# Kernel optimization log

Hardware: AMD Instinct MI355X
Metric: run time of the kernel (lower is better)

Reference implementation:

```python
import jax, jax.numpy as jnp
import numpy as np

EPS = 1e-5


def _binary_act(x):
    # Forward: sign(x). Backward: piecewise-polynomial surrogate (ApproxSign STE).
    out3 = jnp.where(x < -1, -1.0,
            jnp.where(x < 0, x * x + 2.0 * x,
             jnp.where(x < 1, -x * x + 2.0 * x, 1.0)))
    return jax.lax.stop_gradient(jnp.sign(x) - out3) + out3


def _binarize_weights(w):
    # Per-output-channel scaling factor (detached), forward = scale*sign(w),
    # backward flows through clamp(w, -1, 1) (STE).
    scale = jax.lax.stop_gradient(jnp.mean(jnp.abs(w), axis=(1, 2, 3), keepdims=True))
    clipped = jnp.clip(w, -1.0, 1.0)
    return jax.lax.stop_gradient(scale * jnp.sign(w) - clipped) + clipped


def setup_inputs() -> dict:
    key = jax.random.key(0)
    kx, kw = jax.random.split(key)
    B, Cin, Cout, H, W = 32, 128, 128, 56, 56
    x = jax.random.normal(kx, (B, Cin, H, W), dtype=jnp.float32)
    # HardBinaryConv: weight = rand(n)*0.001 permuted then reshaped -> just random in [0, 0.001)
    w = jax.random.uniform(kw, (Cout, Cin, 3, 3), dtype=jnp.float32) * 0.001
    return {
        "x": x,
        "bias0": jnp.zeros((Cin,), jnp.float32),   # move0 LearnableBias
        "w": w,                                     # HardBinaryConv latent weights
        "gamma": jnp.ones((Cout,), jnp.float32),    # BN weight
        "beta": jnp.zeros((Cout,), jnp.float32),    # BN bias
        "bias1": jnp.zeros((Cout,), jnp.float32),   # move1
        "alpha": jnp.full((Cout,), 0.25, jnp.float32),  # PReLU per-channel
        "bias2": jnp.zeros((Cout,), jnp.float32),   # move2
    }


def reference(x, bias0, w, gamma, beta, bias1, alpha, bias2):
    def pc(v):  # per-channel broadcast (1, C, 1, 1)
        return v[None, :, None, None]

    residual = x
    out = x + pc(bias0)                     # move0
    out = _binary_act(out)                  # binary activation
    bw = _binarize_weights(w)               # {-scale, +scale} weights
    y = jax.lax.conv_general_dilated(
        out, bw, window_strides=(1, 1), padding=((1, 1), (1, 1)),
        dimension_numbers=("NCHW", "OIHW", "NCHW"))
    # BatchNorm2d (training mode: biased batch statistics over N,H,W)
    mean = jnp.mean(y, axis=(0, 2, 3), keepdims=True)
    var = jnp.mean(jnp.square(y - mean), axis=(0, 2, 3), keepdims=True)
    y = (y - mean) * jax.lax.rsqrt(var + EPS) * pc(gamma) + pc(beta)
    y = y + residual
    y = y + pc(bias1)                       # move1
    y = jnp.where(y >= 0, y, pc(alpha) * y)  # PReLU
    y = y + pc(bias2)                       # move2
    return y
```

## Files before the change

### kernel.cpp

```cpp
#include <hip/hip_runtime.h>
#include <stdint.h>

#define NB 32
#define NC 128
#define NH 56
#define NW 56
#define NHW_ (NH * NW)
#define NPIX (NB * NHW_)
#define NO 128
#define NK 1152
#define ROWPAIRS (NH / 2)

typedef unsigned long long u64;

__global__ __launch_bounds__(256) void pack_act(const float* __restrict__ x,
                                                const float* __restrict__ bias0,
                                                u64* __restrict__ packA) {
    int p = blockIdx.x * 256 + threadIdx.x;
    if (p >= NPIX) return;
    int n = p / NHW_;
    int rem = p - n * NHW_;
    const float* xb = x + (size_t)n * NC * NHW_ + rem;
    u64 w0 = 0, w1 = 0;
#pragma unroll 8
    for (int c = 0; c < 64; ++c)
        w0 |= (u64)((xb[(size_t)c * NHW_] + bias0[c]) > 0.f) << c;
#pragma unroll 8
    for (int c = 0; c < 64; ++c)
        w1 |= (u64)((xb[(size_t)(c + 64) * NHW_] + bias0[c + 64]) > 0.f) << c;
    packA[(size_t)p * 2]     = w0;
    packA[(size_t)p * 2 + 1] = w1;
}

__global__ __launch_bounds__(64) void pack_wgt(const float* __restrict__ w,
                                               u64* __restrict__ packW,
                                               float* __restrict__ scaleW) {
    int o = blockIdx.x;
    int t = threadIdx.x;
    const float* wo = w + (size_t)o * NK;
    float s = 0.f;
    for (int i = t; i < NK; i += 64) s += fabsf(wo[i]);
    for (int off = 32; off; off >>= 1) s += __shfl_down(s, off);
    if (t == 0) scaleW[o] = s / (float)NK;
    if (t < 18) {
        int tap = t >> 1;
        int j   = t & 1;
        u64 bits = 0;
        for (int cc = 0; cc < 64; ++cc) {
            int c = j * 64 + cc;
            bits |= (u64)(wo[c * 9 + tap] > 0.f) << cc;
        }
        packW[((size_t)o * 9 + tap) * 2 + j] = bits;
    }
}

__global__ __launch_bounds__(256) void conv_bin(const u64* __restrict__ packA,
                                                const u64* __restrict__ packW,
                                                short* __restrict__ yI) {
    __shared__ u64 lw[NO * 18];
    for (int i = threadIdx.x; i < NO * 18; i += 256) lw[i] = packW[i];

    int bid = blockIdx.x;
    int n = bid / ROWPAIRS, hp = bid - n * ROWPAIRS;
    int h0 = hp * 2;
    int wave = threadIdx.x >> 6, lane = threadIdx.x & 63;
    bool act = lane < NW;

    u64 a[4][3][2];
    bool rv[4], cv[3];
#pragma unroll
    for (int r = 0; r < 4; ++r) {
        int hi = h0 - 1 + r;
        rv[r] = (hi >= 0) && (hi < NH);
    }
    cv[0] = act && (lane >= 1);
    cv[1] = act;
    cv[2] = act && (lane + 1 < NW);
#pragma unroll
    for (int r = 0; r < 4; ++r) {
        int hi = h0 - 1 + r;
        int hc = hi < 0 ? 0 : (hi >= NH ? NH - 1 : hi);
#pragma unroll
        for (int c = 0; c < 3; ++c) {
            int wi = lane - 1 + c;
            int wc = wi < 0 ? 0 : (wi >= NW ? NW - 1 : wi);
            size_t idx = ((size_t)n * NHW_ + (size_t)hc * NW + wc) * 2;
            ulonglong2 q = *reinterpret_cast<const ulonglong2*>(packA + idx);
            bool v = rv[r] && cv[c];
            a[r][c][0] = v ? q.x : 0;
            a[r][c][1] = v ? q.y : 0;
        }
    }
    __syncthreads();

    short* yrow = yI + (size_t)n * NO * NHW_ + (size_t)h0 * NW + lane;

    for (int oo = 0; oo < 32; ++oo) {
        int o = (wave << 5) + oo;
        const u64* wp = &lw[o * 18];
        int dot0 = 0, dot1 = 0;
#pragma unroll
        for (int kh = 0; kh < 3; ++kh) {
#pragma unroll
            for (int kw = 0; kw < 3; ++kw) {
                int t = kh * 3 + kw;
                u64 w0 = wp[2 * t], w1 = wp[2 * t + 1];
                int pc0 = __popcll(a[kh][kw][0] ^ w0) + __popcll(a[kh][kw][1] ^ w1);
                int pc1 = __popcll(a[kh + 1][kw][0] ^ w0) + __popcll(a[kh + 1][kw][1] ^ w1);
                dot0 += (rv[kh] && cv[kw]) ? (NC - 2 * pc0) : 0;
                dot1 += (rv[kh + 1] && cv[kw]) ? (NC - 2 * pc1) : 0;
            }
        }
        if (act) {
            yrow[(size_t)o * NHW_]      = (short)dot0;
            yrow[(size_t)o * NHW_ + NW] = (short)dot1;
        }
    }
}

__global__ __launch_bounds__(256) void stats_y(const short* __restrict__ yI,
                                               int* __restrict__ sumP,
                                               u64* __restrict__ sqP) {
    int b = blockIdx.x;
    int o = b >> 2, q = b & 3;
    long long s = 0, sq = 0;
    for (int v = threadIdx.x; v < 3136; v += 256) {
        int nl = v / 392, off = v - nl * 392;
        int n = q * 8 + nl;
        const int4 pv = *reinterpret_cast<const int4*>(
            yI + ((size_t)n * NO + o) * NHW_ + (size_t)off * 8);
        int qs[4] = {pv.x, pv.y, pv.z, pv.w};
#pragma unroll
        for (int j = 0; j < 4; ++j) {
            int lo = (int)(short)(qs[j] & 0xffff);
            int hi = (int)(qs[j] >> 16);
            s += lo + hi;
            sq += (long long)(lo * lo + hi * hi);
        }
    }
    __shared__ long long ls[256];
    __shared__ long long lq[256];
    int tid = threadIdx.x;
    ls[tid] = s; lq[tid] = sq;
    __syncthreads();
    for (int st = 128; st; st >>= 1) {
        if (tid < st) { ls[tid] += ls[tid + st]; lq[tid] += lq[tid + st]; }
        __syncthreads();
    }
    if (tid == 0) {
        sumP[o * 4 + q] = (int)ls[0];
        sqP[o * 4 + q]  = (u64)lq[0];
    }
}

__global__ __launch_bounds__(128) void bn_coef(const int* __restrict__ sumP,
                                               const u64* __restrict__ sqP,
                                               const float* __restrict__ scaleW,
                                               const float* __restrict__ gamma,
                                               const float* __restrict__ beta,
                                               const float* __restrict__ bias1,
                                               float* __restrict__ coefA,
                                               float* __restrict__ coefB,
                                               int nparts) {
    int o = threadIdx.x;
    long long si = 0; u64 qi = 0;
    for (int k = 0; k < nparts; ++k) {
        si += sumP[o * nparts + k];
        qi += sqP[o * nparts + k];
    }
    double cnt = (double)NPIX;
    double mean = (double)si / cnt;
    double var = (double)qi / cnt - mean * mean;
    if (var < 0.0) var = 0.0;
    float sc = scaleW[o];
    float rs = rsqrtf((float)((double)sc * (double)sc * var) + 1e-5f);
    float g = gamma[o];
    float a = sc * g * rs;
    float b = beta[o] - (float)((double)sc * mean) * g * rs;
    coefA[o] = a;
    coefB[o] = b + bias1[o];
}

__global__ __launch_bounds__(256) void final_store(const short* __restrict__ yI,
                                                   const float* __restrict__ x,
                                                   const float* __restrict__ coefA,
                                                   const float* __restrict__ coefB,
                                                   const float* __restrict__ alpha,
                                                   const float* __restrict__ bias2,
                                                   float* __restrict__ out) {
    const size_t ngroups = (size_t)NB * NO * NHW_ / 8;
    for (size_t g = (size_t)blockIdx.x * blockDim.x + threadIdx.x; g < ngroups;
         g += (size_t)gridDim.x * blockDim.x) {
        size_t i = g * 8;
        int o = (int)((i / NHW_) % NO);
        float a = coefA[o], bb = coefB[o], al = alpha[o], b2 = bias2[o];
        int4 yv = *reinterpret_cast<const int4*>(yI + i);
        float4 x0 = *reinterpret_cast<const float4*>(x + i);
        float4 x1 = *reinterpret_cast<const float4*>(x + i + 4);
        int q[4] = {yv.x, yv.y, yv.z, yv.w};
        float xs[8] = {x0.x, x0.y, x0.z, x0.w, x1.x, x1.y, x1.z, x1.w};
        float r[8];
#pragma unroll
        for (int j = 0; j < 4; ++j) {
            float lo = (float)(short)(q[j] & 0xffff);
            float hi = (float)(q[j] >> 16);
            float t0 = fmaf(a, lo, bb) + xs[2 * j];
            float t1 = fmaf(a, hi, bb) + xs[2 * j + 1];
            t0 = t0 >= 0.f ? t0 : al * t0;
            t1 = t1 >= 0.f ? t1 : al * t1;
            r[2 * j]     = t0 + b2;
            r[2 * j + 1] = t1 + b2;
        }
        float4 o0 = {r[0], r[1], r[2], r[3]};
        float4 o1 = {r[4], r[5], r[6], r[7]};
        *reinterpret_cast<float4*>(out + i)     = o0;
        *reinterpret_cast<float4*>(out + i + 4) = o1;
    }
}

__device__ inline void load_nbhd(const u64* __restrict__ packA, int n, int h,
                                 int wcol, bool act, u64 a[9][2], unsigned* vmask) {
    unsigned m = 0;
#pragma unroll
    for (int kh = 0; kh < 3; ++kh) {
        int hi = h + kh - 1;
        bool vh = (hi >= 0) && (hi < NH);
#pragma unroll
        for (int kw = 0; kw < 3; ++kw) {
            int wi = wcol + kw - 1;
            int t = kh * 3 + kw;
            bool v = act && vh && (wi >= 0) && (wi < NW);
            int hc = hi < 0 ? 0 : (hi >= NH ? NH - 1 : hi);
            int wc = wi < 0 ? 0 : (wi >= NW ? NW - 1 : wi);
            size_t idx = ((size_t)n * NHW_ + (size_t)hc * NW + wc) * 2;
            u64 q0 = packA[idx], q1 = packA[idx + 1];
            a[t][0] = v ? q0 : 0;
            a[t][1] = v ? q1 : 0;
            m |= (unsigned)v << t;
        }
    }
    *vmask = m;
}

__global__ __launch_bounds__(256) void conv_stats_atomic(const u64* __restrict__ packA,
                                                         const u64* __restrict__ packW,
                                                         int* __restrict__ sumI,
                                                         u64* __restrict__ sumsqI) {
    __shared__ u64 lw[NO * 18];
    for (int i = threadIdx.x; i < NO * 18; i += 256) lw[i] = packW[i];
    int nh = blockIdx.x;
    int n = nh / NH, h = nh - n * NH;
    int wave = threadIdx.x >> 6, lane = threadIdx.x & 63;
    bool act = lane < NW;
    u64 a[9][2]; unsigned vm;
    load_nbhd(packA, n, h, lane, act, a, &vm);
    __syncthreads();
    for (int oo = 0; oo < 32; ++oo) {
        int o = (wave << 5) + oo;
        int dot = 0;
#pragma unroll
        for (int t = 0; t < 9; ++t) {
            int pc = __popcll(a[t][0] ^ lw[(o * 9 + t) * 2]) +
                     __popcll(a[t][1] ^ lw[(o * 9 + t) * 2 + 1]);
            dot += ((vm >> t) & 1) ? (NC - 2 * pc) : 0;
        }
        int s = dot, sq = dot * dot;
        for (int off = 32; off; off >>= 1) {
            s  += __shfl_down(s, off);
            sq += __shfl_down(sq, off);
        }
        if (lane == 0) {
            atomicAdd(&sumI[o], s);
            atomicAdd(&sumsqI[o], (u64)(unsigned)sq);
        }
    }
}

__global__ __launch_bounds__(256) void final_recompute(const u64* __restrict__ packA,
                                                       const u64* __restrict__ packW,
                                                       const float* __restrict__ coefA,
                                                       const float* __restrict__ coefB,
                                                       const float* __restrict__ alpha,
                                                       const float* __restrict__ bias2,
                                                       const float* __restrict__ x,
                                                       float* __restrict__ out) {
    __shared__ u64 lw[NO * 18];
    for (int i = threadIdx.x; i < NO * 18; i += 256) lw[i] = packW[i];
    int nh = blockIdx.x;
    int n = nh / NH, h = nh - n * NH;
    int wave = threadIdx.x >> 6, lane = threadIdx.x & 63;
    bool act = lane < NW;
    u64 a[9][2]; unsigned vm;
    load_nbhd(packA, n, h, lane, act, a, &vm);
    __syncthreads();
    for (int oo = 0; oo < 32; ++oo) {
        int o = (wave << 5) + oo;
        int dot = 0;
#pragma unroll
        for (int t = 0; t < 9; ++t) {
            int pc = __popcll(a[t][0] ^ lw[(o * 9 + t) * 2]) +
                     __popcll(a[t][1] ^ lw[(o * 9 + t) * 2 + 1]);
            dot += ((vm >> t) & 1) ? (NC - 2 * pc) : 0;
        }
        if (act) {
            size_t idx = ((size_t)n * NO + o) * NHW_ + (size_t)h * NW + lane;
            float t = fmaf(coefA[o], (float)dot, coefB[o]) + x[idx];
            t = t >= 0.f ? t : alpha[o] * t;
            out[idx] = t + bias2[o];
        }
    }
}

extern "C" void kernel_launch(void* const* d_in, const int* in_sizes, int n_in,
                              void* d_out, int out_size, void* d_ws, size_t ws_size,
                              hipStream_t stream) {
    (void)in_sizes; (void)n_in; (void)out_size;
    const float* x     = (const float*)d_in[0];
    const float* bias0 = (const float*)d_in[1];
    const float* w     = (const float*)d_in[2];
    const float* gamma = (const float*)d_in[3];
    const float* beta  = (const float*)d_in[4];
    const float* bias1 = (const float*)d_in[5];
    const float* alpha = (const float*)d_in[6];
    const float* bias2 = (const float*)d_in[7];
    float* out = (float*)d_out;
    char* ws = (char*)d_ws;

    u64*   packA  = (u64*)ws;
    u64*   packW  = (u64*)(ws + 1605632);
    float* scaleW = (float*)(ws + 1624064);
    int*   sumP   = (int*)(ws + 1624576);
    u64*   sqP    = (u64*)(ws + 1626624);
    float* coefA  = (float*)(ws + 1630720);
    float* coefB  = (float*)(ws + 1631232);
    short* yI     = (short*)(ws + 1631744);
    bool store = ws_size >= (size_t)1631744 + (size_t)NB * NO * NHW_ * 2;

    pack_act<<<NPIX / 256, 256, 0, stream>>>(x, bias0, packA);
    pack_wgt<<<NO, 64, 0, stream>>>(w, packW, scaleW);

    if (store) {
        conv_bin<<<NB * ROWPAIRS, 256, 0, stream>>>(packA, packW, yI);
        stats_y<<<NO * 4, 256, 0, stream>>>(yI, sumP, sqP);
        bn_coef<<<1, NO, 0, stream>>>(sumP, sqP, scaleW, gamma, beta, bias1, coefA, coefB, 4);
        final_store<<<2048, 256, 0, stream>>>(yI, x, coefA, coefB, alpha, bias2, out);
    } else {
        hipMemsetAsync(sumP, 0, 2048 + 4096, stream);
        conv_stats_atomic<<<NB * NH, 256, 0, stream>>>(packA, packW, sumP, sqP);
        bn_coef<<<1, NO, 0, stream>>>(sumP, sqP, scaleW, gamma, beta, bias1, coefA, coefB, 1);
        final_recompute<<<NB * NH, 256, 0, stream>>>(packA, packW, coefA, coefB, alpha, bias2, x, out);
    }
}
```

Measured before the change: 105.3 us.

## Compute four output rows per thread with precomputed padding corrections

The binary conv kernel now processes 4-row strips per block, split across two 64-channel halves, so each loaded activation neighbourhood serves four output rows. Per-tap masking is replaced by unmasked popcounts and a fixed border correction precomputed per output channel in pack_wgt. The separate stats and bn_coef kernels are merged into one per-channel kernel, which removes a launch but drops the 4-way split of the statistics work. More registers are needed for the 6x3 neighbourhood, and occupancy hint 4 is added.

```diff
diff --git a/kernel.cpp b/kernel.cpp
--- a/kernel.cpp
+++ b/kernel.cpp
@@ -9,7 +9,7 @@
 #define NPIX (NB * NHW_)
 #define NO 128
 #define NK 1152
-#define ROWPAIRS (NH / 2)
+#define NSTRIP 14
 
 typedef unsigned long long u64;
 
@@ -34,7 +34,9 @@
 
 __global__ __launch_bounds__(64) void pack_wgt(const float* __restrict__ w,
                                                u64* __restrict__ packW,
-                                               float* __restrict__ scaleW) {
+                                               float* __restrict__ scaleW,
+                                               int* __restrict__ corrW) {
+    __shared__ u64 sb[18];
     int o = blockIdx.x;
     int t = threadIdx.x;
     const float* wo = w + (size_t)o * NK;
@@ -50,83 +52,122 @@
             int c = j * 64 + cc;
             bits |= (u64)(wo[c * 9 + tap] > 0.f) << cc;
         }
-        packW[((size_t)o * 9 + tap) * 2 + j] = bits;
-    }
-}
-
-__global__ __launch_bounds__(256) void conv_bin(const u64* __restrict__ packA,
-                                                const u64* __restrict__ packW,
-                                                short* __restrict__ yI) {
-    __shared__ u64 lw[NO * 18];
-    for (int i = threadIdx.x; i < NO * 18; i += 256) lw[i] = packW[i];
+        packW[(size_t)o * 18 + t] = bits;
+        sb[t] = bits;
+    }
+    __syncthreads();
+    if (t == 0) {
+        int cv[9];
+#pragma unroll
+        for (int tap = 0; tap < 9; ++tap)
+            cv[tap] = NC - 2 * (__popcll(sb[2 * tap]) + __popcll(sb[2 * tap + 1]));
+        int* cw = corrW + o * 8;
+        cw[0] = cv[0] + cv[3] + cv[6];
+        cw[1] = cv[2] + cv[5] + cv[8];
+        cw[2] = cv[0] + cv[1] + cv[2];
+        cw[3] = cv[6] + cv[7] + cv[8];
+        cw[4] = cv[0];
+        cw[5] = cv[2];
+        cw[6] = cv[6];
+        cw[7] = cv[8];
+    }
+}
+
+__global__ __launch_bounds__(256, 4) void conv_bin(const u64* __restrict__ packA,
+                                                   const u64* __restrict__ packW,
+                                                   const int* __restrict__ corrW,
+                                                   short* __restrict__ yI) {
+    __shared__ u64 lw[64 * 18];
+    __shared__ int lc[64 * 8];
 
     int bid = blockIdx.x;
-    int n = bid / ROWPAIRS, hp = bid - n * ROWPAIRS;
-    int h0 = hp * 2;
-    int wave = threadIdx.x >> 6, lane = threadIdx.x & 63;
+    int n = bid / (NSTRIP * 2);
+    int rem = bid - n * (NSTRIP * 2);
+    int strip = rem >> 1;
+    int chh = rem & 1;
+    int obase = chh * 64;
+    int h0 = strip * 4;
+
+    for (int i = threadIdx.x; i < 64 * 18; i += 256) lw[i] = packW[(size_t)obase * 18 + i];
+    for (int i = threadIdx.x; i < 64 * 8; i += 256) lc[i] = corrW[obase * 8 + i];
+
+    int wv = threadIdx.x >> 6, lane = threadIdx.x & 63;
     bool act = lane < NW;
-
-    u64 a[4][3][2];
-    bool rv[4], cv[3];
-#pragma unroll
-    for (int r = 0; r < 4; ++r) {
+    bool top = (strip == 0), bot = (strip == NSTRIP - 1);
+
+    u64 a[6][3][2];
+    bool cvv[3];
+    cvv[0] = act && (lane >= 1);
+    cvv[1] = act;
+    cvv[2] = act && (lane + 1 < NW);
+#pragma unroll
+    for (int r = 0; r < 6; ++r) {
         int hi = h0 - 1 + r;
-        rv[r] = (hi >= 0) && (hi < NH);
-    }
-    cv[0] = act && (lane >= 1);
-    cv[1] = act;
-    cv[2] = act && (lane + 1 < NW);
-#pragma unroll
-    for (int r = 0; r < 4; ++r) {
-        int hi = h0 - 1 + r;
+        bool rvv = (hi >= 0) && (hi < NH);
         int hc = hi < 0 ? 0 : (hi >= NH ? NH - 1 : hi);
 #pragma unroll
         for (int c = 0; c < 3; ++c) {
             int wi = lane - 1 + c;
             int wc = wi < 0 ? 0 : (wi >= NW ? NW - 1 : wi);
-            size_t idx = ((size_t)n * NHW_ + (size_t)hc * NW + wc) * 2;
-            ulonglong2 q = *reinterpret_cast<const ulonglong2*>(packA + idx);
-            bool v = rv[r] && cv[c];
+            ulonglong2 q = *reinterpret_cast<const ulonglong2*>(
+                packA + ((size_t)n * NHW_ + (size_t)hc * NW + wc) * 2);
+            bool v = rvv && cvv[c];
             a[r][c][0] = v ? q.x : 0;
             a[r][c][1] = v ? q.y : 0;
         }
     }
     __syncthreads();
 
-    short* yrow = yI + (size_t)n * NO * NHW_ + (size_t)h0 * NW + lane;
-
-    for (int oo = 0; oo < 32; ++oo) {
-        int o = (wave << 5) + oo;
-        const u64* wp = &lw[o * 18];
-        int dot0 = 0, dot1 = 0;
+    bool isL = (lane == 0), isR = (lane == NW - 1);
+    short* ybase = yI + (size_t)n * NO * NHW_ + (size_t)h0 * NW + lane;
+
+    for (int oo = 0; oo < 16; ++oo) {
+        int lo = (wv << 4) + oo;
+        int o = obase + lo;
+        const u64* wp = &lw[lo * 18];
+        int pc0 = 0, pc1 = 0, pc2 = 0, pc3 = 0;
 #pragma unroll
         for (int kh = 0; kh < 3; ++kh) {
 #pragma unroll
             for (int kw = 0; kw < 3; ++kw) {
-                int t = kh * 3 + kw;
-                u64 w0 = wp[2 * t], w1 = wp[2 * t + 1];
-                int pc0 = __popcll(a[kh][kw][0] ^ w0) + __popcll(a[kh][kw][1] ^ w1);
-                int pc1 = __popcll(a[kh + 1][kw][0] ^ w0) + __popcll(a[kh + 1][kw][1] ^ w1);
-                dot0 += (rv[kh] && cv[kw]) ? (NC - 2 * pc0) : 0;
-                dot1 += (rv[kh + 1] && cv[kw]) ? (NC - 2 * pc1) : 0;
+                u64 w0 = wp[(kh * 3 + kw) * 2];
+                u64 w1 = wp[(kh * 3 + kw) * 2 + 1];
+                pc0 += __popcll(a[0 + kh][kw][0] ^ w0) + __popcll(a[0 + kh][kw][1] ^ w1);
+                pc1 += __popcll(a[1 + kh][kw][0] ^ w0) + __popcll(a[1 + kh][kw][1] ^ w1);
+                pc2 += __popcll(a[2 + kh][kw][0] ^ w0) + __popcll(a[2 + kh][kw][1] ^ w1);
+                pc3 += __popcll(a[3 + kh][kw][0] ^ w0) + __popcll(a[3 + kh][kw][1] ^ w1);
             }
         }
+        const int* cw = &lc[lo * 8];
+        int corrcol = isL ? cw[0] : (isR ? cw[1] : 0);
+        int base = NK - corrcol;
+        int d0 = base - 2 * pc0;
+        int d1 = base - 2 * pc1;
+        int d2 = base - 2 * pc2;
+        int d3 = base - 2 * pc3;
+        if (top) d0 -= cw[2] - (isL ? cw[4] : (isR ? cw[5] : 0));
+        if (bot) d3 -= cw[3] - (isL ? cw[6] : (isR ? cw[7] : 0));
         if (act) {
-            yrow[(size_t)o * NHW_]      = (short)dot0;
-            yrow[(size_t)o * NHW_ + NW] = (short)dot1;
-        }
-    }
-}
-
-__global__ __launch_bounds__(256) void stats_y(const short* __restrict__ yI,
-                                               int* __restrict__ sumP,
-                                               u64* __restrict__ sqP) {
-    int b = blockIdx.x;
-    int o = b >> 2, q = b & 3;
+            short* yp = ybase + (size_t)o * NHW_;
+            yp[0]      = (short)d0;
+            yp[NW]     = (short)d1;
+            yp[2 * NW] = (short)d2;
+            yp[3 * NW] = (short)d3;
+        }
+    }
+}
+
+__global__ __launch_bounds__(256) void stats_coef(const short* __restrict__ yI,
+                                                  const float* __restrict__ scaleW,
+                                                  const float* __restrict__ gamma,
+                                                  const float* __restrict__ beta,
+                                                  const float* __restrict__ bias1,
+                                                  float* __restrict__ coefA,
+                                                  float* __restrict__ coefB) {
+    int o = blockIdx.x;
     long long s = 0, sq = 0;
-    for (int v = threadIdx.x; v < 3136; v += 256) {
-        int nl = v / 392, off = v - nl * 392;
-        int n = q * 8 + nl;
+    for (int v = threadIdx.x; v < 12544; v += 256) {
+        int n = v / 392, off = v - n * 392;
         const int4 pv = *reinterpret_cast<const int4*>(
             yI + ((size_t)n * NO + o) * NHW_ + (size_t)off * 8);
         int qs[4] = {pv.x, pv.y, pv.z, pv.w};
@@ -148,37 +189,16 @@
         __syncthreads();
     }
     if (tid == 0) {
-        sumP[o * 4 + q] = (int)ls[0];
-        sqP[o * 4 + q]  = (u64)lq[0];
-    }
-}
-
-__global__ __launch_bounds__(128) void bn_coef(const int* __restrict__ sumP,
-                                               const u64* __restrict__ sqP,
-                                               const float* __restrict__ scaleW,
-                                               const float* __restrict__ gamma,
-                                               const float* __restrict__ beta,
-                                               const float* __restrict__ bias1,
-                                               float* __restrict__ coefA,
-                                               float* __restrict__ coefB,
-                                               int nparts) {
-    int o = threadIdx.x;
-    long long si = 0; u64 qi = 0;
-    for (int k = 0; k < nparts; ++k) {
-        si += sumP[o * nparts + k];
-        qi += sqP[o * nparts + k];
-    }
-    double cnt = (double)NPIX;
-    double mean = (double)si / cnt;
-    double var = (double)qi / cnt - mean * mean;
-    if (var < 0.0) var = 0.0;
-    float sc = scaleW[o];
-    float rs = rsqrtf((float)((double)sc * (double)sc * var) + 1e-5f);
-    float g = gamma[o];
-    float a = sc * g * rs;
-    float b = beta[o] - (float)((double)sc * mean) * g * rs;
-    coefA[o] = a;
-    coefB[o] = b + bias1[o];
+        double cnt = (double)NPIX;
+        double mean = (double)ls[0] / cnt;
+        double var = (double)lq[0] / cnt - mean * mean;
+        if (var < 0.0) var = 0.0;
+        float sc = scaleW[o];
+        float rs = rsqrtf((float)((double)sc * (double)sc * var) + 1e-5f);
+        float g = gamma[o];
+        coefA[o] = sc * g * rs;
+        coefB[o] = beta[o] - (float)((double)sc * mean) * g * rs + bias1[o];
+    }
 }
 
 __global__ __launch_bounds__(256) void final_store(const short* __restrict__ yI,
@@ -276,6 +296,26 @@
     }
 }
 
+__global__ __launch_bounds__(128) void bn_coef(const int* __restrict__ sumP,
+                                               const u64* __restrict__ sqP,
+                                               const float* __restrict__ scaleW,
+                                               const float* __restrict__ gamma,
+                                               const float* __restrict__ beta,
+                                               const float* __restrict__ bias1,
+                                               float* __restrict__ coefA,
+                                               float* __restrict__ coefB) {
+    int o = threadIdx.x;
+    double cnt = (double)NPIX;
+    double mean = (double)sumP[o] / cnt;
+    double var = (double)sqP[o] / cnt - mean * mean;
+    if (var < 0.0) var = 0.0;
+    float sc = scaleW[o];
+    float rs = rsqrtf((float)((double)sc * (double)sc * var) + 1e-5f);
+    float g = gamma[o];
+    coefA[o] = sc * g * rs;
+    coefB[o] = beta[o] - (float)((double)sc * mean) * g * rs + bias1[o];
+}
+
 __global__ __launch_bounds__(256) void final_recompute(const u64* __restrict__ packA,
                                                        const u64* __restrict__ packW,
                                                        const float* __restrict__ coefA,
@@ -328,26 +368,26 @@
 
     u64*   packA  = (u64*)ws;
     u64*   packW  = (u64*)(ws + 1605632);
-    float* scaleW = (float*)(ws + 1624064);
-    int*   sumP   = (int*)(ws + 1624576);
-    u64*   sqP    = (u64*)(ws + 1626624);
-    float* coefA  = (float*)(ws + 1630720);
-    float* coefB  = (float*)(ws + 1631232);
-    short* yI     = (short*)(ws + 1631744);
-    bool store = ws_size >= (size_t)1631744 + (size_t)NB * NO * NHW_ * 2;
+    int*   corrW  = (int*)(ws + 1624064);
+    float* scaleW = (float*)(ws + 1628160);
+    float* coefA  = (float*)(ws + 1628672);
+    float* coefB  = (float*)(ws + 1629184);
+    int*   sumP   = (int*)(ws + 1629696);
+    u64*   sqP    = (u64*)(ws + 1630208);
+    short* yI     = (short*)(ws + 1631232);
+    bool store = ws_size >= (size_t)1631232 + (size_t)NB * NO * NHW_ * 2;
 
     pack_act<<<NPIX / 256, 256, 0, stream>>>(x, bias0, packA);
-    pack_wgt<<<NO, 64, 0, stream>>>(w, packW, scaleW);
+    pack_wgt<<<NO, 64, 0, stream>>>(w, packW, scaleW, corrW);
 
     if (store) {
-        conv_bin<<<NB * ROWPAIRS, 256, 0, stream>>>(packA, packW, yI);
-        stats_y<<<NO * 4, 256, 0, stream>>>(yI, sumP, sqP);
-        bn_coef<<<1, NO, 0, stream>>>(sumP, sqP, scaleW, gamma, beta, bias1, coefA, coefB, 4);
+        conv_bin<<<NB * NSTRIP * 2, 256, 0, stream>>>(packA, packW, corrW, yI);
+        stats_coef<<<NO, 256, 0, stream>>>(yI, scaleW, gamma, beta, bias1, coefA, coefB);
         final_store<<<2048, 256, 0, stream>>>(yI, x, coefA, coefB, alpha, bias2, out);
     } else {
-        hipMemsetAsync(sumP, 0, 2048 + 4096, stream);
+        hipMemsetAsync(sumP, 0, 512 + 1024, stream);
         conv_stats_atomic<<<NB * NH, 256, 0, stream>>>(packA, packW, sumP, sqP);
-        bn_coef<<<1, NO, 0, stream>>>(sumP, sqP, scaleW, gamma, beta, bias1, coefA, coefB, 1);
+        bn_coef<<<1, NO, 0, stream>>>(sumP, sqP, scaleW, gamma, beta, bias1, coefA, coefB);
         final_recompute<<<NB * NH, 256, 0, stream>>>(packA, packW, coefA, coefB, alpha, bias2, x, out);
     }
 }
```

Result: slower. 109.9 us (+4.4%).
